# Optimization experiments

Measured on AMD Instinct MI355X. Metric: run time of the kernel, lower is better.

## Reference

```python
import jax, jax.numpy as jnp
import numpy as np

B, S, D = 8, 2048, 1024
PADDING_IDX = 0
NEG_BIG = -1000000000.0


def setup_inputs() -> dict:
    key = jax.random.key(0)
    k1, k2, k3 = jax.random.split(key, 3)
    state = jax.random.normal(k1, (B, S, D), dtype=jnp.float32)
    x = jax.random.normal(k2, (B, S, D), dtype=jnp.float32)
    src = jax.random.randint(k3, (B, S), 0, 5, dtype=jnp.int64)
    return {"state": state, "x": x, "src": src}


def reference(state, x, src):
    # mask: True at padding positions, shape [B, S]
    mask = src == PADDING_IDX
    # scores[b,s,t] = <state[b,s], x[b,t]>
    scores = jnp.einsum("bsd,btd->bst", state, x)
    scores = jnp.where(mask[:, :, None], NEG_BIG, scores)
    # softmax over the source (s) axis, dim=-2
    p_attn = jax.nn.softmax(scores, axis=-2)  # [B, S, T]
    # w = (state^T @ p_attn)^T -> [B, T, D]
    w = jnp.einsum("bsd,bst->btd", state, p_attn)
    # in-place mask: rows at padding positions set to -inf (T == S here)
    w = jnp.where(mask[:, :, None], -jnp.inf, w)
    attn_score = jax.nn.softmax(w, axis=1)  # softmax over T per feature
    # out = (state^T @ attn_score)^T -> [B, D, D]
    out = jnp.einsum("bsd,bse->bed", state, attn_score)
    return out
```

## Files before the change

kernel.cpp:

```cpp
#include <hip/hip_runtime.h>
#include <hip/hip_bf16.h>

#define SS 2048
#define TT 2048
#define DD 1024
#define NB 8

typedef __attribute__((ext_vector_type(8))) short short8v;
typedef __attribute__((ext_vector_type(8))) unsigned short us8;
typedef __attribute__((ext_vector_type(4))) unsigned short us4;
typedef __attribute__((ext_vector_type(4))) float f32x4;

__device__ __forceinline__ float bf2f(unsigned short u) {
    union { unsigned int i; float f; } v; v.i = ((unsigned int)u) << 16; return v.f;
}
__device__ __forceinline__ unsigned short f2bf(float f) {
    union { float f; unsigned int i; } v; v.f = f;
    unsigned int x = v.i;
    return (unsigned short)((x + 0x7fffu + ((x >> 16) & 1u)) >> 16);
}

__global__ __launch_bounds__(256) void conv_k(
    const float* __restrict__ in, unsigned short* __restrict__ outv, size_t n)
{
    size_t i = ((size_t)blockIdx.x * 256 + threadIdx.x) * 8;
    const size_t stride = (size_t)gridDim.x * 256 * 8;
    for (; i < n; i += stride) {
        float4 a = *reinterpret_cast<const float4*>(in + i);
        float4 b = *reinterpret_cast<const float4*>(in + i + 4);
        us8 o;
        o[0] = f2bf(a.x); o[1] = f2bf(a.y); o[2] = f2bf(a.z); o[3] = f2bf(a.w);
        o[4] = f2bf(b.x); o[5] = f2bf(b.y); o[6] = f2bf(b.z); o[7] = f2bf(b.w);
        *reinterpret_cast<us8*>(outv + i) = o;
    }
}

__global__ __launch_bounds__(256) void transpose_k(
    const float* __restrict__ in, unsigned short* __restrict__ outT,
    unsigned short* __restrict__ outB, size_t sIn, size_t sOutT, size_t sOutB)
{
    __shared__ float t[64][65];
    const int g = blockIdx.z;
    const float* I = in + g * sIn;
    unsigned short* OT = outT + g * sOutT;
    unsigned short* OB = outB + g * sOutB;
    const int s0 = blockIdx.x * 64, d0 = blockIdx.y * 64;
    const int tid = threadIdx.x;
    #pragma unroll
    for (int i = 0; i < 4; ++i) {
        int slot = tid + i * 256;
        int rr = slot >> 4, rc = (slot & 15) * 4;
        float4 v = *reinterpret_cast<const float4*>(I + (size_t)(s0 + rr) * DD + d0 + rc);
        t[rr][rc + 0] = v.x; t[rr][rc + 1] = v.y; t[rr][rc + 2] = v.z; t[rr][rc + 3] = v.w;
        us4 o; o[0] = f2bf(v.x); o[1] = f2bf(v.y); o[2] = f2bf(v.z); o[3] = f2bf(v.w);
        *reinterpret_cast<us4*>(OB + (size_t)(s0 + rr) * DD + d0 + rc) = o;
    }
    __syncthreads();
    #pragma unroll
    for (int i = 0; i < 4; ++i) {
        int slot = tid + i * 256;
        int dr = slot >> 4, sidx = (slot & 15) * 4;
        us4 o;
        #pragma unroll
        for (int j = 0; j < 4; ++j) o[j] = f2bf(t[sidx + j][dr]);
        *reinterpret_cast<us4*>(OT + (size_t)(d0 + dr) * SS + s0 + sidx) = o;
    }
}

template<int OUT_F32>
__global__ __launch_bounds__(512, 2) void gemm256(
    const unsigned short* __restrict__ A, const unsigned short* __restrict__ B,
    void* __restrict__ C, int lda, int ldb, int ldc, int K,
    size_t sA, size_t sB, size_t sC)
{
    __shared__ unsigned short As[2][256 * 64];
    __shared__ unsigned short Bs[2][256 * 64];

    const int nxy = gridDim.x * gridDim.y;
    const int nwg = nxy * gridDim.z;
    int wg = blockIdx.x + gridDim.x * (blockIdx.y + gridDim.y * blockIdx.z);
    if ((nwg & 7) == 0) {
        const int cpx = nwg >> 3;
        wg = (wg & 7) * cpx + (wg >> 3);
    }
    const int g  = wg / nxy;
    const int rm = wg - g * nxy;
    const int by = rm / gridDim.x;
    const int bx = rm - by * gridDim.x;

    const unsigned short* Ag = A + g * sA;
    const unsigned short* Bg = B + g * sB;
    const int m0 = by * 256, n0 = bx * 256;
    const int tid = threadIdx.x, lane = tid & 63, wid = tid >> 6;
    const int wr = wid >> 2, wc = wid & 3;
    const int lr = lane & 15, lkc = lane >> 4;
    const int strow = tid >> 3;
    const int stsp = tid & 7;

    f32x4 acc[8][4] = {};
    const int NT = K >> 6;

#define STAGE256(buf, kt)                                                       \
    {                                                                           \
        const int k0 = (kt) << 6;                                               \
        _Pragma("unroll")                                                       \
        for (int j = 0; j < 4; ++j) {                                           \
            int r = j * 64 + strow;                                             \
            int c = stsp ^ (r & 7);                                             \
            __builtin_amdgcn_global_load_lds(                                   \
                (const __attribute__((address_space(1))) unsigned int*)        \
                    (Ag + (size_t)(m0 + r) * lda + k0 + c * 8),                 \
                (__attribute__((address_space(3))) unsigned int*)              \
                    (&As[buf][j * 4096 + wid * 512]),                           \
                16, 0, 0);                                                      \
        }                                                                       \
        _Pragma("unroll")                                                       \
        for (int j = 0; j < 4; ++j) {                                           \
            int r = j * 64 + strow;                                             \
            int c = stsp ^ (r & 7);                                             \
            __builtin_amdgcn_global_load_lds(                                   \
                (const __attribute__((address_space(1))) unsigned int*)        \
                    (Bg + (size_t)(n0 + r) * ldb + k0 + c * 8),                 \
                (__attribute__((address_space(3))) unsigned int*)              \
                    (&Bs[buf][j * 4096 + wid * 512]),                           \
                16, 0, 0);                                                      \
        }                                                                       \
    }

    int cur = 0;
    STAGE256(0, 0);
    __syncthreads();
    for (int kt = 0; kt < NT; ++kt) {
        if (kt + 1 < NT) STAGE256(cur ^ 1, kt + 1);
        #pragma unroll
        for (int ksub = 0; ksub < 2; ++ksub) {
            const int c0 = ksub * 4 + lkc;
            short8v a[8], bb[4];
            #pragma unroll
            for (int mi = 0; mi < 8; ++mi) {
                int r = wr * 128 + mi * 16 + lr;
                a[mi] = *reinterpret_cast<const short8v*>(
                    &As[cur][r * 64 + ((c0 ^ (r & 7)) * 8)]);
            }
            #pragma unroll
            for (int ni = 0; ni < 4; ++ni) {
                int r = wc * 64 + ni * 16 + lr;
                bb[ni] = *reinterpret_cast<const short8v*>(
                    &Bs[cur][r * 64 + ((c0 ^ (r & 7)) * 8)]);
            }
            #pragma unroll
            for (int ni = 0; ni < 4; ++ni)
                #pragma unroll
                for (int mi = 0; mi < 8; ++mi)
                    acc[mi][ni] = __builtin_amdgcn_mfma_f32_16x16x32_bf16(a[mi], bb[ni], acc[mi][ni], 0, 0, 0);
        }
        __syncthreads();
        cur ^= 1;
    }
#undef STAGE256

    const int orow = (lane >> 4) * 4, ocol = lane & 15;
    if (OUT_F32) {
        float* Cg = (float*)C + g * sC;
        #pragma unroll
        for (int mi = 0; mi < 8; ++mi)
            #pragma unroll
            for (int ni = 0; ni < 4; ++ni)
                #pragma unroll
                for (int r = 0; r < 4; ++r)
                    Cg[(size_t)(m0 + wr * 128 + mi * 16 + orow + r) * ldc + (n0 + wc * 64 + ni * 16 + ocol)] = acc[mi][ni][r];
    } else {
        unsigned short* Cg = (unsigned short*)C + g * sC;
        #pragma unroll
        for (int mi = 0; mi < 8; ++mi)
            #pragma unroll
            for (int ni = 0; ni < 4; ++ni)
                #pragma unroll
                for (int r = 0; r < 4; ++r)
                    Cg[(size_t)(m0 + wr * 128 + mi * 16 + orow + r) * ldc + (n0 + wc * 64 + ni * 16 + ocol)] = f2bf(acc[mi][ni][r]);
    }
}

template<int OUT_F32>
__global__ __launch_bounds__(256, 4) void gemm_nt(
    const unsigned short* __restrict__ A, const unsigned short* __restrict__ B,
    void* __restrict__ C, int lda, int ldb, int ldc, int K,
    size_t sA, size_t sB, size_t sC)
{
    __shared__ unsigned short As[2][128 * 32];
    __shared__ unsigned short Bs[2][128 * 32];

    const int nxy = gridDim.x * gridDim.y;
    const int nwg = nxy * gridDim.z;
    int wg = blockIdx.x + gridDim.x * (blockIdx.y + gridDim.y * blockIdx.z);
    if ((nwg & 7) == 0) {
        const int cpx = nwg >> 3;
        wg = (wg & 7) * cpx + (wg >> 3);
    }
    const int g  = wg / nxy;
    const int rm = wg - g * nxy;
    const int by = rm / gridDim.x;
    const int bx = rm - by * gridDim.x;

    const unsigned short* Ag = A + g * sA;
    const unsigned short* Bg = B + g * sB;
    const int m0 = by * 128, n0 = bx * 128;
    const int tid = threadIdx.x, lane = tid & 63, wid = tid >> 6;
    const int wm = (wid >> 1) * 64, wn = (wid & 1) * 64;
    const int lr16 = lane & 15, lk = lane >> 4;
    const int sr = wid * 32 + (lane >> 2);
    const int sp = lane & 3;

    f32x4 acc[4][4] = {};
    const int NT = K >> 5;

#define STAGE(buf, kt)                                                          \
    {                                                                           \
        const int k0 = (kt) << 5;                                               \
        _Pragma("unroll")                                                       \
        for (int j = 0; j < 2; ++j) {                                           \
            int r = sr + j * 16;                                                \
            int c = sp ^ ((r >> 1) & 3);                                        \
            __builtin_amdgcn_global_load_lds(                                   \
                (const __attribute__((address_space(1))) unsigned int*)        \
                    (Ag + (size_t)(m0 + r) * lda + k0 + c * 8),                 \
                (__attribute__((address_space(3))) unsigned int*)              \
                    (&As[buf][(wid * 32 + j * 16) * 32]),                       \
                16, 0, 0);                                                      \
            __builtin_amdgcn_global_load_lds(                                   \
                (const __attribute__((address_space(1))) unsigned int*)        \
                    (Bg + (size_t)(n0 + r) * ldb + k0 + c * 8),                 \
                (__attribute__((address_space(3))) unsigned int*)              \
                    (&Bs[buf][(wid * 32 + j * 16) * 32]),                       \
                16, 0, 0);                                                      \
        }                                                                       \
    }

    int cur = 0;
    STAGE(0, 0);
    __syncthreads();
    for (int kt = 0; kt < NT; ++kt) {
        if (kt + 1 < NT) STAGE(cur ^ 1, kt + 1);
        short8v a[4], bb[4];
        #pragma unroll
        for (int mi = 0; mi < 4; ++mi) {
            int r = wm + mi * 16 + lr16;
            a[mi] = *reinterpret_cast<const short8v*>(
                &As[cur][r * 32 + (lk ^ ((r >> 1) & 3)) * 8]);
        }
        #pragma unroll
        for (int ni = 0; ni < 4; ++ni) {
            int r = wn + ni * 16 + lr16;
            bb[ni] = *reinterpret_cast<const short8v*>(
                &Bs[cur][r * 32 + (lk ^ ((r >> 1) & 3)) * 8]);
        }
        #pragma unroll
        for (int ni = 0; ni < 4; ++ni)
            #pragma unroll
            for (int mi = 0; mi < 4; ++mi)
                acc[mi][ni] = __builtin_amdgcn_mfma_f32_16x16x32_bf16(a[mi], bb[ni], acc[mi][ni], 0, 0, 0);
        __syncthreads();
        cur ^= 1;
    }
#undef STAGE

    const int orow = (lane >> 4) * 4, ocol = lane & 15;
    if (OUT_F32) {
        float* Cg = (float*)C + g * sC;
        #pragma unroll
        for (int mi = 0; mi < 4; ++mi)
            #pragma unroll
            for (int ni = 0; ni < 4; ++ni)
                #pragma unroll
                for (int r = 0; r < 4; ++r)
                    Cg[(size_t)(m0 + wm + mi * 16 + orow + r) * ldc + (n0 + wn + ni * 16 + ocol)] = acc[mi][ni][r];
    } else {
        unsigned short* Cg = (unsigned short*)C + g * sC;
        #pragma unroll
        for (int mi = 0; mi < 4; ++mi)
            #pragma unroll
            for (int ni = 0; ni < 4; ++ni)
                #pragma unroll
                for (int r = 0; r < 4; ++r)
                    Cg[(size_t)(m0 + wm + mi * 16 + orow + r) * ldc + (n0 + wn + ni * 16 + ocol)] = f2bf(acc[mi][ni][r]);
    }
}

__global__ __launch_bounds__(256) void softmax1_k(
    unsigned short* __restrict__ P, const float* __restrict__ x,
    const float* __restrict__ state, const int* __restrict__ src,
    int b0, size_t sP)
{
    const int t = blockIdx.x, g = blockIdx.y, b = b0 + g, tid = threadIdx.x;
    const int lane = tid & 63, wid = tid >> 6;
    unsigned short* row = P + g * sP + (size_t)t * SS;
    const int* sb = src + (size_t)b * SS;
    __shared__ float redA[4], redB[4];
    __shared__ int cnt, list[96];
    __shared__ float corr[96];

    us8 rv = *reinterpret_cast<const us8*>(row + tid * 8);
    int4 mk0 = reinterpret_cast<const int4*>(sb)[tid * 2];
    int4 mk1 = reinterpret_cast<const int4*>(sb)[tid * 2 + 1];
    int msk[8] = { mk0.x == 0, mk0.y == 0, mk0.z == 0, mk0.w == 0,
                   mk1.x == 0, mk1.y == 0, mk1.z == 0, mk1.w == 0 };
    float v[8];
    float m = -1e30f;
    #pragma unroll
    for (int i = 0; i < 8; ++i) {
        v[i] = msk[i] ? -1e30f : bf2f(rv[i]);
        m = fmaxf(m, v[i]);
    }
    #pragma unroll
    for (int o = 32; o > 0; o >>= 1) m = fmaxf(m, __shfl_xor(m, o, 64));
    if (lane == 0) redA[wid] = m;
    if (tid == 0) cnt = 0;
    __syncthreads();
    const float M = fmaxf(fmaxf(redA[0], redA[1]), fmaxf(redA[2], redA[3]));
    #pragma unroll
    for (int i = 0; i < 8; ++i) {
        if (!msk[i] && v[i] > M - 16.f) {
            int j = atomicAdd(&cnt, 1);
            if (j < 96) list[j] = tid * 8 + i;
        }
    }
    __syncthreads();
    const int n = min(cnt, 96);
    const float* xr = x + (size_t)b * SS * DD + (size_t)t * DD;
    float4 xa[4];
    #pragma unroll
    for (int c = 0; c < 4; ++c) xa[c] = reinterpret_cast<const float4*>(xr)[lane + c * 64];
    for (int j = wid; j < n; j += 4) {
        const float* sr = state + (size_t)b * SS * DD + (size_t)list[j] * DD;
        float p = 0.f;
        #pragma unroll
        for (int c = 0; c < 4; ++c) {
            float4 c4 = reinterpret_cast<const float4*>(sr)[lane + c * 64];
            p += xa[c].x * c4.x + xa[c].y * c4.y + xa[c].z * c4.z + xa[c].w * c4.w;
        }
        #pragma unroll
        for (int o = 32; o > 0; o >>= 1) p += __shfl_xor(p, o, 64);
        if (lane == 0) corr[j] = p;
    }
    __syncthreads();
    for (int j = 0; j < n; ++j) {
        int s = list[j];
        if ((s >> 3) == tid) v[s & 7] = corr[j];
    }
    float m2 = -1e30f;
    #pragma unroll
    for (int i = 0; i < 8; ++i) m2 = fmaxf(m2, v[i]);
    #pragma unroll
    for (int o = 32; o > 0; o >>= 1) m2 = fmaxf(m2, __shfl_xor(m2, o, 64));
    if (lane == 0) redA[wid] = m2;
    __syncthreads();
    const float M2 = fmaxf(fmaxf(redA[0], redA[1]), fmaxf(redA[2], redA[3]));
    float l = 0.f;
    #pragma unroll
    for (int i = 0; i < 8; ++i) if (!msk[i]) { v[i] = __expf(v[i] - M2); l += v[i]; }
    #pragma unroll
    for (int o = 32; o > 0; o >>= 1) l += __shfl_xor(l, o, 64);
    if (lane == 0) redB[wid] = l;
    __syncthreads();
    const float inv = 1.f / (redB[0] + redB[1] + redB[2] + redB[3]);
    us8 ov;
    #pragma unroll
    for (int i = 0; i < 8; ++i) ov[i] = msk[i] ? 0 : f2bf(v[i] * inv);
    *reinterpret_cast<us8*>(row + tid * 8) = ov;
}

__global__ __launch_bounds__(256) void softmax2_k(
    const unsigned short* __restrict__ wT, unsigned short* __restrict__ attnT,
    const int* __restrict__ src, int b0, size_t sW, size_t sAt)
{
    const int e = blockIdx.x, g = blockIdx.y, b = b0 + g, tid = threadIdx.x;
    const int lane = tid & 63, wid = tid >> 6;
    const unsigned short* row = wT + g * sW + (size_t)e * TT;
    unsigned short* orow = attnT + g * sAt + (size_t)e * TT;
    const int* sb = src + (size_t)b * SS;
    __shared__ float shm[4], shl[4];
    us8 rv = *reinterpret_cast<const us8*>(row + tid * 8);
    int4 mk0 = reinterpret_cast<const int4*>(sb)[tid * 2];
    int4 mk1 = reinterpret_cast<const int4*>(sb)[tid * 2 + 1];
    int msk[8] = { mk0.x == 0, mk0.y == 0, mk0.z == 0, mk0.w == 0,
                   mk1.x == 0, mk1.y == 0, mk1.z == 0, mk1.w == 0 };
    float v[8];
    float m = -1e30f;
    #pragma unroll
    for (int i = 0; i < 8; ++i) {
        v[i] = msk[i] ? -1e30f : bf2f(rv[i]);
        m = fmaxf(m, v[i]);
    }
    #pragma unroll
    for (int o = 32; o > 0; o >>= 1) m = fmaxf(m, __shfl_xor(m, o, 64));
    if (lane == 0) shm[wid] = m;
    __syncthreads();
    const float M = fmaxf(fmaxf(shm[0], shm[1]), fmaxf(shm[2], shm[3]));
    float l = 0.f;
    #pragma unroll
    for (int i = 0; i < 8; ++i) if (!msk[i]) { v[i] = __expf(v[i] - M); l += v[i]; }
    #pragma unroll
    for (int o = 32; o > 0; o >>= 1) l += __shfl_xor(l, o, 64);
    if (lane == 0) shl[wid] = l;
    __syncthreads();
    const float inv = 1.f / (shl[0] + shl[1] + shl[2] + shl[3]);
    us8 ov;
    #pragma unroll
    for (int i = 0; i < 8; ++i) ov[i] = msk[i] ? 0 : f2bf(v[i] * inv);
    *reinterpret_cast<us8*>(orow + tid * 8) = ov;
}

extern "C" void kernel_launch(void* const* d_in, const int* in_sizes, int n_in,
                              void* d_out, int out_size, void* d_ws, size_t ws_size,
                              hipStream_t stream)
{
    const float* state = (const float*)d_in[0];
    const float* x     = (const float*)d_in[1];
    const int* src     = (const int*)d_in[2];
    float* out         = (float*)d_out;

    const size_t SD = (size_t)SS * DD;
    const size_t perP  = (size_t)SS * TT * 2;
    const size_t perST = (size_t)DD * SS * 2;
    const size_t perW  = (size_t)DD * TT * 2;
    const size_t perXB = (size_t)SS * DD * 2;
    const size_t perSB = (size_t)SS * DD * 2;
    const size_t perBatch = perP + perST + perW + perXB + perSB;

    int G = 8;
    while (G > 1 && (size_t)G * perBatch > ws_size) G >>= 1;

    char* base = (char*)d_ws;
    unsigned short* P  = (unsigned short*)base;
    unsigned short* ST = (unsigned short*)(base + (size_t)G * perP);
    unsigned short* W  = (unsigned short*)(base + (size_t)G * (perP + perST));
    unsigned short* XB = (unsigned short*)(base + (size_t)G * (perP + perST + perW));
    unsigned short* SB = (unsigned short*)(base + (size_t)G * (perP + perST + perW + perXB));

    const size_t sP  = (size_t)SS * TT;
    const size_t sST = (size_t)DD * SS;
    const size_t sW  = (size_t)DD * TT;
    const size_t sXB = (size_t)SS * DD;

    for (int b0 = 0; b0 < NB; b0 += G) {
        conv_k<<<2048, 256, 0, stream>>>(x + (size_t)b0 * SD, XB, (size_t)G * SD);
        transpose_k<<<dim3(SS / 64, DD / 64, G), 256, 0, stream>>>(
            state + (size_t)b0 * SD, ST, SB, SD, sST, sXB);

        gemm256<0><<<dim3(SS / 256, TT / 256, G), 512, 0, stream>>>(
            XB, SB, P, DD, DD, SS, DD, sXB, sXB, sP);

        softmax1_k<<<dim3(TT, G), 256, 0, stream>>>(P, x, state, src, b0, sP);

        gemm256<0><<<dim3(TT / 256, DD / 256, G), 512, 0, stream>>>(
            ST, P, W, SS, SS, TT, SS, sST, sP, sW);

        softmax2_k<<<dim3(DD, G), 256, 0, stream>>>(W, P, src, b0, sW, sP);

        gemm_nt<1><<<dim3(DD / 128, DD / 128, G), 256, 0, stream>>>(
            P, ST, out + (size_t)b0 * DD * DD, TT, SS, DD, TT, sP, sST, (size_t)DD * DD);
    }
}
```

Measured before the change: 328.7 us.

## Restructure GEMM main loop into quadrant-staged ping-pong pipeline with barriers and priorities

Replaces the simple double-buffered k-loop in the 256x256 GEMM with a finer-grained schedule. Global-to-LDS loads are split into half-tile A/B quadrants and interleaved with LDS reads and 16-MFMA clusters, separated by explicit barriers, with s_setprio raised during MFMA bursts and manual vmcnt waits. Launch bounds drop to one block per SM, which frees registers for the preloaded fragments. The goal is to hide memory latency behind MFMA work, at the cost of more barriers and reliance on exact vmcnt accounting. It also assumes NT is even.

```diff
diff --git a/kernel.cpp b/kernel.cpp
--- a/kernel.cpp
+++ b/kernel.cpp
@@ -68,7 +68,7 @@
 }
 
 template<int OUT_F32>
-__global__ __launch_bounds__(512, 2) void gemm256(
+__global__ __launch_bounds__(512, 1) void gemm256(
     const unsigned short* __restrict__ A, const unsigned short* __restrict__ B,
     void* __restrict__ C, int lda, int ldb, int ldc, int K,
     size_t sA, size_t sB, size_t sC)
@@ -94,70 +94,115 @@
     const int tid = threadIdx.x, lane = tid & 63, wid = tid >> 6;
     const int wr = wid >> 2, wc = wid & 3;
     const int lr = lane & 15, lkc = lane >> 4;
-    const int strow = tid >> 3;
-    const int stsp = tid & 7;
 
     f32x4 acc[8][4] = {};
+    short8v a[4][2], b[4][2];
     const int NT = K >> 6;
 
-#define STAGE256(buf, kt)                                                       \
+#define BARX { asm volatile("" ::: "memory"); __builtin_amdgcn_s_barrier(); asm volatile("" ::: "memory"); }
+
+#define STAGE_A(d, mq, kt)                                                      \
     {                                                                           \
-        const int k0 = (kt) << 6;                                               \
+        const int k0_ = (kt) << 6;                                              \
         _Pragma("unroll")                                                       \
-        for (int j = 0; j < 4; ++j) {                                           \
-            int r = j * 64 + strow;                                             \
-            int c = stsp ^ (r & 7);                                             \
+        for (int j = 0; j < 2; ++j) {                                           \
+            int rb = j * 128 + (mq) * 64 + wid * 8;                             \
+            int r = rb + (lane >> 3);                                           \
+            int c = (lane & 7) ^ (r & 7);                                       \
             __builtin_amdgcn_global_load_lds(                                   \
                 (const __attribute__((address_space(1))) unsigned int*)        \
-                    (Ag + (size_t)(m0 + r) * lda + k0 + c * 8),                 \
+                    (Ag + (size_t)(m0 + r) * lda + k0_ + c * 8),                \
                 (__attribute__((address_space(3))) unsigned int*)              \
-                    (&As[buf][j * 4096 + wid * 512]),                           \
+                    (&As[d][rb * 64]),                                          \
                 16, 0, 0);                                                      \
         }                                                                       \
+    }
+
+#define STAGE_B(d, nq, kt)                                                      \
+    {                                                                           \
+        const int k0_ = (kt) << 6;                                              \
         _Pragma("unroll")                                                       \
-        for (int j = 0; j < 4; ++j) {                                           \
-            int r = j * 64 + strow;                                             \
-            int c = stsp ^ (r & 7);                                             \
+        for (int j = 0; j < 2; ++j) {                                           \
+            int rb = (j * 2 + (wid >> 2)) * 64 + (nq) * 32 + (wid & 3) * 8;     \
+            int r = rb + (lane >> 3);                                           \
+            int c = (lane & 7) ^ (r & 7);                                       \
             __builtin_amdgcn_global_load_lds(                                   \
                 (const __attribute__((address_space(1))) unsigned int*)        \
-                    (Bg + (size_t)(n0 + r) * ldb + k0 + c * 8),                 \
+                    (Bg + (size_t)(n0 + r) * ldb + k0_ + c * 8),                \
                 (__attribute__((address_space(3))) unsigned int*)              \
-                    (&Bs[buf][j * 4096 + wid * 512]),                           \
+                    (&Bs[d][rb * 64]),                                          \
                 16, 0, 0);                                                      \
         }                                                                       \
     }
 
-    int cur = 0;
-    STAGE256(0, 0);
-    __syncthreads();
-    for (int kt = 0; kt < NT; ++kt) {
-        if (kt + 1 < NT) STAGE256(cur ^ 1, kt + 1);
-        #pragma unroll
-        for (int ksub = 0; ksub < 2; ++ksub) {
-            const int c0 = ksub * 4 + lkc;
-            short8v a[8], bb[4];
-            #pragma unroll
-            for (int mi = 0; mi < 8; ++mi) {
-                int r = wr * 128 + mi * 16 + lr;
-                a[mi] = *reinterpret_cast<const short8v*>(
-                    &As[cur][r * 64 + ((c0 ^ (r & 7)) * 8)]);
-            }
-            #pragma unroll
-            for (int ni = 0; ni < 4; ++ni) {
-                int r = wc * 64 + ni * 16 + lr;
-                bb[ni] = *reinterpret_cast<const short8v*>(
-                    &Bs[cur][r * 64 + ((c0 ^ (r & 7)) * 8)]);
-            }
-            #pragma unroll
-            for (int ni = 0; ni < 4; ++ni)
-                #pragma unroll
-                for (int mi = 0; mi < 8; ++mi)
-                    acc[mi][ni] = __builtin_amdgcn_mfma_f32_16x16x32_bf16(a[mi], bb[ni], acc[mi][ni], 0, 0, 0);
-        }
-        __syncthreads();
-        cur ^= 1;
-    }
-#undef STAGE256
+#define DS_A(d, mq)                                                             \
+    {                                                                           \
+        _Pragma("unroll")                                                       \
+        for (int i = 0; i < 4; ++i) {                                           \
+            int r = wr * 128 + (mq) * 64 + i * 16 + lr;                         \
+            _Pragma("unroll")                                                   \
+            for (int ks = 0; ks < 2; ++ks)                                      \
+                a[i][ks] = *reinterpret_cast<const short8v*>(                   \
+                    &As[d][r * 64 + (((ks * 4 + lkc) ^ (r & 7)) << 3)]);        \
+        }                                                                       \
+    }
+
+#define DS_B(d, nq)                                                             \
+    {                                                                           \
+        _Pragma("unroll")                                                       \
+        for (int i = 0; i < 2; ++i) {                                           \
+            int r = wc * 64 + (nq) * 32 + i * 16 + lr;                          \
+            _Pragma("unroll")                                                   \
+            for (int ks = 0; ks < 2; ++ks)                                      \
+                b[(nq) * 2 + i][ks] = *reinterpret_cast<const short8v*>(        \
+                    &Bs[d][r * 64 + (((ks * 4 + lkc) ^ (r & 7)) << 3)]);        \
+        }                                                                       \
+    }
+
+#define MFMA16(mq, nq)                                                          \
+    {                                                                           \
+        __builtin_amdgcn_s_setprio(1);                                          \
+        _Pragma("unroll")                                                       \
+        for (int i = 0; i < 4; ++i)                                             \
+            _Pragma("unroll")                                                   \
+            for (int i2 = 0; i2 < 2; ++i2)                                      \
+                _Pragma("unroll")                                               \
+                for (int ks = 0; ks < 2; ++ks)                                  \
+                    acc[(mq) * 4 + i][(nq) * 2 + i2] =                          \
+                        __builtin_amdgcn_mfma_f32_16x16x32_bf16(                \
+                            a[i][ks], b[(nq) * 2 + i2][ks],                     \
+                            acc[(mq) * 4 + i][(nq) * 2 + i2], 0, 0, 0);         \
+        __builtin_amdgcn_s_setprio(0);                                          \
+    }
+
+    STAGE_A(0, 0, 0); STAGE_B(0, 0, 0); STAGE_A(0, 1, 0); STAGE_B(0, 1, 0);
+    STAGE_A(1, 0, 1); STAGE_B(1, 0, 1);
+    asm volatile("s_waitcnt vmcnt(4)" ::: "memory");
+    BARX;
+
+    for (int it = 0; it < (NT >> 1); ++it) {
+        const int T0 = 2 * it, T1 = 2 * it + 1;
+        const int S0 = (T0 + 2 < NT) ? T0 + 2 : T0;
+        const int S1 = (T1 + 2 < NT) ? T1 + 2 : T1;
+        STAGE_A(1, 1, T1); DS_A(0, 0); DS_B(0, 0); BARX; MFMA16(0, 0); BARX;
+        STAGE_B(1, 1, T1); DS_B(0, 1); BARX; MFMA16(0, 1); BARX;
+        STAGE_A(0, 0, S0); DS_A(0, 1); BARX; MFMA16(1, 0); BARX;
+        STAGE_B(0, 0, S0); BARX; MFMA16(1, 1);
+        asm volatile("s_waitcnt vmcnt(4)" ::: "memory"); BARX;
+        STAGE_A(0, 1, S0); DS_A(1, 0); DS_B(1, 0); BARX; MFMA16(0, 0); BARX;
+        STAGE_B(0, 1, S0); DS_B(1, 1); BARX; MFMA16(0, 1); BARX;
+        STAGE_A(1, 0, S1); DS_A(1, 1); BARX; MFMA16(1, 0); BARX;
+        STAGE_B(1, 0, S1); BARX; MFMA16(1, 1);
+        asm volatile("s_waitcnt vmcnt(4)" ::: "memory"); BARX;
+    }
+    asm volatile("s_waitcnt vmcnt(0)" ::: "memory");
+
+#undef BARX
+#undef STAGE_A
+#undef STAGE_B
+#undef DS_A
+#undef DS_B
+#undef MFMA16
 
     const int orow = (lane >> 4) * 4, ocol = lane & 15;
     if (OUT_F32) {
```

Measured after the change: 348.2 us. 5.9% more time.
